# Optimization experiments

Hardware: AMD Instinct MI355X
Metric: run time of the kernel (lower is better)

Reference implementation:

```python
import math
import jax, jax.numpy as jnp
import numpy as np

B, S, H, N = 2, 2048, 2048, 16
HN = H // N
ALPHA = 32.0
MASK_VALUE = 10000.0


def setup_inputs() -> dict:
    key = jax.random.key(0)
    k1, k2, k3, k4, k5 = jax.random.split(key, 5)
    hidden_states = jax.random.normal(k1, (B, S, H), dtype=jnp.float32)
    # causal (left-to-right) multiplicative mask, broadcastable to [b, n, s, s]
    ltor_mask = jnp.tril(jnp.ones((S, S), dtype=jnp.float32))[None, None, :, :]
    # torch Linear params: y = x @ W.T + b
    w_qkv = jax.random.normal(k2, (3 * H, H), dtype=jnp.float32) * (1.0 / math.sqrt(H))
    b_qkv = jnp.zeros((3 * H,), dtype=jnp.float32)
    w_dense = jax.random.normal(k3, (H, H), dtype=jnp.float32) * (1.0 / math.sqrt(H))
    b_dense = jnp.zeros((H,), dtype=jnp.float32)
    return {"hidden_states": hidden_states, "ltor_mask": ltor_mask,
            "w_qkv": w_qkv, "b_qkv": b_qkv, "w_dense": w_dense, "b_dense": b_dense}


def reference(hidden_states, ltor_mask, w_qkv, b_qkv, w_dense, b_dense):
    b, s, h = hidden_states.shape
    # fused qkv projection
    qkv = hidden_states @ w_qkv.T + b_qkv                       # [b, s, 3h]
    q, k, v = jnp.split(qkv, 3, axis=-1)

    def heads(t):  # [b, s, h] -> [b, n, s, hn]
        return t.reshape(b, s, N, HN).transpose(0, 2, 1, 3)

    q, k, v = heads(q), heads(k), heads(v)
    # cogview pb_relax: scale query before matmul
    scores = jnp.einsum('bnsd,bntd->bnst', q / math.sqrt(HN), k)  # [b, n, s, s]
    m = ltor_mask[:, :, -s:]
    scores = scores * m - MASK_VALUE * (1.0 - m)
    # pb_relax max stabilization: per (batch, head) global max of scores/alpha
    scaled = scores / ALPHA
    maxes = jax.lax.stop_gradient(jnp.max(scaled, axis=(-2, -1), keepdims=True))
    scores = (scaled - maxes) * ALPHA
    probs = jax.nn.softmax(scores, axis=-1)
    ctx = jnp.einsum('bnst,bntd->bnsd', probs, v)                # [b, n, s, hn]
    ctx = ctx.transpose(0, 2, 1, 3).reshape(b, s, h)
    out = ctx @ w_dense.T + b_dense
    return out
```

## Files before the change

### kernel.cpp

```cpp
#include <hip/hip_runtime.h>

typedef __bf16 bf16_t;
typedef __bf16 bf16x8 __attribute__((ext_vector_type(8)));
typedef __bf16 bf16x4 __attribute__((ext_vector_type(4)));
typedef float f32x4 __attribute__((ext_vector_type(4)));

#define MFMA16(a, b, c) __builtin_amdgcn_mfma_f32_16x16x32_bf16((a), (b), (c), 0, 0, 0)

__device__ __forceinline__ void gload_lds16(const void* g, void* l) {
  __builtin_amdgcn_global_load_lds(
      (__attribute__((address_space(1))) void*)(g),
      (__attribute__((address_space(3))) void*)(l), 16, 0, 0);
}

__device__ __forceinline__ void block_bar() {
  asm volatile("" ::: "memory");
  __builtin_amdgcn_s_barrier();
  asm volatile("" ::: "memory");
}

__global__ __launch_bounds__(256) void cvt_f32_bf16(const float* __restrict__ in,
                                                    bf16_t* __restrict__ out, int n4) {
  int i = blockIdx.x * 256 + threadIdx.x;
  if (i >= n4) return;
  float4 v = ((const float4*)in)[i];
  bf16x4 o;
  o[0] = (bf16_t)v.x; o[1] = (bf16_t)v.y; o[2] = (bf16_t)v.z; o[3] = (bf16_t)v.w;
  ((bf16x4*)out)[i] = o;
}

template <int EPI>
__global__ __launch_bounds__(256) void gemm_bt(
    const bf16_t* __restrict__ A, const bf16_t* __restrict__ Bw,
    const float* __restrict__ bias,
    void* __restrict__ o0, void* __restrict__ o1, void* __restrict__ o2,
    int M, int N, int K) {
  __shared__ __attribute__((aligned(16))) bf16_t As[2][128][32];
  __shared__ __attribute__((aligned(16))) bf16_t Bs[2][128][32];
  const int tid = threadIdx.x;
  const int lane = tid & 63, wave = tid >> 6;
  const int wr = (wave >> 1) * 64, wc = (wave & 1) * 64;
  const int l15 = lane & 15, l4 = lane >> 4;
  const int bm = blockIdx.y * 128, bn = blockIdx.x * 128;

  f32x4 acc[4][4];
#pragma unroll
  for (int i = 0; i < 4; ++i)
#pragma unroll
    for (int j = 0; j < 4; ++j)
#pragma unroll
      for (int r = 0; r < 4; ++r) acc[i][j][r] = 0.0f;

  const int r0 = tid >> 2;
  const int co = (tid & 3) * 8;
  const bf16_t* gA = A + (size_t)(bm + r0) * K + co;
  const bf16_t* gB = Bw + (size_t)(bn + r0) * K + co;

  const int nt = K >> 5;

  gload_lds16(gA, &As[0][r0][co]);
  gload_lds16(gA + (size_t)64 * K, &As[0][r0 + 64][co]);
  gload_lds16(gB, &Bs[0][r0][co]);
  gload_lds16(gB + (size_t)64 * K, &Bs[0][r0 + 64][co]);

#pragma unroll 1
  for (int t = 0; t < nt; ++t) {
    const int cb = t & 1;
    if (t + 1 < nt) {
      const int kk = (t + 1) << 5;
      const int nb = cb ^ 1;
      gload_lds16(gA + kk, &As[nb][r0][co]);
      gload_lds16(gA + kk + (size_t)64 * K, &As[nb][r0 + 64][co]);
      gload_lds16(gB + kk, &Bs[nb][r0][co]);
      gload_lds16(gB + kk + (size_t)64 * K, &Bs[nb][r0 + 64][co]);
      asm volatile("s_waitcnt vmcnt(4)" ::: "memory");
    } else {
      asm volatile("s_waitcnt vmcnt(0)" ::: "memory");
    }
    block_bar();
    bf16x8 a[4], b[4];
#pragma unroll
    for (int i = 0; i < 4; ++i) a[i] = *(const bf16x8*)(&As[cb][wr + i * 16 + l15][l4 * 8]);
#pragma unroll
    for (int j = 0; j < 4; ++j) b[j] = *(const bf16x8*)(&Bs[cb][wc + j * 16 + l15][l4 * 8]);
#pragma unroll
    for (int i = 0; i < 4; ++i)
#pragma unroll
      for (int j = 0; j < 4; ++j) acc[i][j] = MFMA16(a[i], b[j], acc[i][j]);
    block_bar();
  }

  if (EPI == 0) {
    bf16_t* qb = (bf16_t*)o0;
    bf16_t* kb = (bf16_t*)o1;
    bf16_t* vtb = (bf16_t*)o2;
    const int which = bn >> 11;
    const int head = (bn & 2047) >> 7;
#pragma unroll
    for (int i = 0; i < 4; ++i)
#pragma unroll
      for (int j = 0; j < 4; ++j)
#pragma unroll
        for (int r = 0; r < 4; ++r) {
          int m = bm + wr + i * 16 + l4 * 4 + r;
          int n = bn + wc + j * 16 + l15;
          float v = acc[i][j][r] + bias[n];
          int b = m >> 11, s = m & 2047;
          int d = n & 127;
          size_t hb = (size_t)(b * 16 + head);
          if (which == 0) {
            v *= 0.08838834764831845f;
            qb[(hb * 2048 + s) * 128 + d] = (bf16_t)v;
          } else if (which == 1) {
            kb[(hb * 2048 + s) * 128 + d] = (bf16_t)v;
          } else {
            vtb[(hb * 128 + d) * 2048 + s] = (bf16_t)v;
          }
        }
  } else {
    float* O = (float*)o0;
#pragma unroll
    for (int i = 0; i < 4; ++i)
#pragma unroll
      for (int j = 0; j < 4; ++j)
#pragma unroll
        for (int r = 0; r < 4; ++r) {
          int m = bm + wr + i * 16 + l4 * 4 + r;
          int n = bn + wc + j * 16 + l15;
          O[(size_t)m * N + n] = acc[i][j][r] + bias[n];
        }
  }
}

__global__ __launch_bounds__(512) void attn_kernel(
    const bf16_t* __restrict__ qbuf, const bf16_t* __restrict__ kbuf,
    const bf16_t* __restrict__ vtbuf, bf16_t* __restrict__ ctx) {
  __shared__ __attribute__((aligned(16))) bf16_t Ks[2][64][128];
  __shared__ __attribute__((aligned(16))) bf16_t Vts[2][128][64];
  __shared__ __attribute__((aligned(16))) bf16_t Ps[8][16][64];

  const int tid = threadIdx.x, lane = tid & 63, w = tid >> 6;
  const int l15 = lane & 15, l4 = lane >> 4;
  const int hb = blockIdx.y;
  const size_t hoff = (size_t)hb * 2048 * 128;
  const bf16_t* qh = qbuf + hoff;
  const bf16_t* kh = kbuf + hoff;
  const bf16_t* vh = vtbuf + hoff;
  const int b = hb >> 4, head = hb & 15;

  const int kr0 = tid >> 4, ks0 = tid & 15;
  const int vr0 = tid >> 3, vs0 = tid & 7;

  int buf = 0;

#pragma unroll 1
  for (int phase = 0; phase < 2; ++phase) {
    const int qt = phase == 0 ? blockIdx.x : 15 - blockIdx.x;
    const int q0 = qt * 128;
    const int nt = 2 * qt + 2;

    bf16x8 qa[4];
#pragma unroll
    for (int ks = 0; ks < 4; ++ks)
      qa[ks] = *(const bf16x8*)(qh + (size_t)(q0 + w * 16 + l15) * 128 + ks * 32 + l4 * 8);

    f32x4 accO[8];
#pragma unroll
    for (int df = 0; df < 8; ++df)
#pragma unroll
      for (int r = 0; r < 4; ++r) accO[df][r] = 0.0f;
    float mrow[4], lrow[4];
#pragma unroll
    for (int r = 0; r < 4; ++r) { mrow[r] = -1e30f; lrow[r] = 0.0f; }

    {
      const int kv0 = 0;
#pragma unroll
      for (int it = 0; it < 2; ++it) {
        int row = kr0 + it * 32, sch = ks0 ^ (row & 7);
        gload_lds16(kh + (size_t)(kv0 + row) * 128 + sch * 8, &Ks[buf][row][ks0 * 8]);
      }
#pragma unroll
      for (int it = 0; it < 2; ++it) {
        int row = vr0 + it * 64, sch = vs0 ^ (row & 7);
        gload_lds16(vh + (size_t)row * 2048 + kv0 + sch * 8, &Vts[buf][row][vs0 * 8]);
      }
    }

#pragma unroll 1
    for (int t = 0; t < nt; ++t) {
      const int kv0 = t * 64;
      if (t + 1 < nt) {
        const int kvn = (t + 1) * 64;
        const int nb = buf ^ 1;
#pragma unroll
        for (int it = 0; it < 2; ++it) {
          int row = kr0 + it * 32, sch = ks0 ^ (row & 7);
          gload_lds16(kh + (size_t)(kvn + row) * 128 + sch * 8, &Ks[nb][row][ks0 * 8]);
        }
#pragma unroll
        for (int it = 0; it < 2; ++it) {
          int row = vr0 + it * 64, sch = vs0 ^ (row & 7);
          gload_lds16(vh + (size_t)row * 2048 + kvn + sch * 8, &Vts[nb][row][vs0 * 8]);
        }
        asm volatile("s_waitcnt vmcnt(4)" ::: "memory");
      } else {
        asm volatile("s_waitcnt vmcnt(0)" ::: "memory");
      }
      block_bar();

      const bool active = (kv0 <= q0 + w * 16 + 15);
      if (active) {
        f32x4 sc[4];
#pragma unroll
        for (int nf = 0; nf < 4; ++nf) {
#pragma unroll
          for (int r = 0; r < 4; ++r) sc[nf][r] = 0.0f;
          int row = nf * 16 + l15;
#pragma unroll
          for (int ks = 0; ks < 4; ++ks) {
            int ch = (ks * 4 + l4) ^ (row & 7);
            bf16x8 kf = *(const bf16x8*)(&Ks[buf][row][ch * 8]);
            sc[nf] = MFMA16(qa[ks], kf, sc[nf]);
          }
        }

        if (kv0 + 63 > q0 + w * 16) {
#pragma unroll
          for (int nf = 0; nf < 4; ++nf)
#pragma unroll
            for (int r = 0; r < 4; ++r) {
              int qi = q0 + w * 16 + l4 * 4 + r;
              int kv = kv0 + nf * 16 + l15;
              if (kv > qi) sc[nf][r] = -1e30f;
            }
        }

        float tmax[4];
#pragma unroll
        for (int r = 0; r < 4; ++r)
          tmax[r] = fmaxf(fmaxf(sc[0][r], sc[1][r]), fmaxf(sc[2][r], sc[3][r]));
#pragma unroll
        for (int msk = 1; msk <= 8; msk <<= 1)
#pragma unroll
          for (int r = 0; r < 4; ++r)
            tmax[r] = fmaxf(tmax[r], __shfl_xor(tmax[r], msk, 64));

        bool defer = __all(tmax[0] <= mrow[0] + 8.0f && tmax[1] <= mrow[1] + 8.0f &&
                           tmax[2] <= mrow[2] + 8.0f && tmax[3] <= mrow[3] + 8.0f);
        if (!defer) {
          float scl[4];
#pragma unroll
          for (int r = 0; r < 4; ++r) {
            float mn = fmaxf(mrow[r], tmax[r]);
            scl[r] = __expf(mrow[r] - mn);
            mrow[r] = mn;
            lrow[r] *= scl[r];
          }
#pragma unroll
          for (int df = 0; df < 8; ++df)
#pragma unroll
            for (int r = 0; r < 4; ++r) accO[df][r] *= scl[r];
        }

        float rsum[4];
#pragma unroll
        for (int r = 0; r < 4; ++r) {
          float s0 = 0.0f;
#pragma unroll
          for (int nf = 0; nf < 4; ++nf) {
            float p = __expf(sc[nf][r] - mrow[r]);
            sc[nf][r] = p;
            s0 += p;
          }
          rsum[r] = s0;
        }
#pragma unroll
        for (int msk = 1; msk <= 8; msk <<= 1)
#pragma unroll
          for (int r = 0; r < 4; ++r) rsum[r] += __shfl_xor(rsum[r], msk, 64);
#pragma unroll
        for (int r = 0; r < 4; ++r) lrow[r] += rsum[r];

#pragma unroll
        for (int nf = 0; nf < 4; ++nf)
#pragma unroll
          for (int r = 0; r < 4; ++r) {
            int qi = l4 * 4 + r;
            int kv = nf * 16 + l15;
            int ch = (kv >> 3) ^ (qi & 7);
            Ps[w][qi][ch * 8 + (kv & 7)] = (bf16_t)sc[nf][r];
          }

        bf16x8 pa[2];
#pragma unroll
        for (int k2 = 0; k2 < 2; ++k2) {
          int ch = (k2 * 4 + l4) ^ (l15 & 7);
          pa[k2] = *(const bf16x8*)(&Ps[w][l15][ch * 8]);
        }
#pragma unroll
        for (int df = 0; df < 8; ++df) {
          int row = df * 16 + l15;
#pragma unroll
          for (int k2 = 0; k2 < 2; ++k2) {
            int ch = (k2 * 4 + l4) ^ (row & 7);
            bf16x8 vf = *(const bf16x8*)(&Vts[buf][row][ch * 8]);
            accO[df] = MFMA16(pa[k2], vf, accO[df]);
          }
        }
      }
      block_bar();
      buf ^= 1;
    }

    float inv[4];
#pragma unroll
    for (int r = 0; r < 4; ++r) inv[r] = 1.0f / lrow[r];
#pragma unroll
    for (int df = 0; df < 8; ++df)
#pragma unroll
      for (int r = 0; r < 4; ++r) {
        int s = q0 + w * 16 + l4 * 4 + r;
        int col = head * 128 + df * 16 + l15;
        ctx[((size_t)(b * 2048 + s)) * 2048 + col] = (bf16_t)(accO[df][r] * inv[r]);
      }
  }
}

extern "C" void kernel_launch(void* const* d_in, const int* in_sizes, int n_in,
                              void* d_out, int out_size, void* d_ws, size_t ws_size,
                              hipStream_t stream) {
  const float* hs = (const float*)d_in[0];
  const float* w_qkv = (const float*)d_in[2];
  const float* b_qkv = (const float*)d_in[3];
  const float* w_dense = (const float*)d_in[4];
  const float* b_dense = (const float*)d_in[5];
  float* out = (float*)d_out;

  const size_t SZ_HS = (size_t)4096 * 2048;
  const size_t SZ_WQKV = (size_t)6144 * 2048;
  const size_t SZ_WD = (size_t)2048 * 2048;
  const size_t SZ_H = (size_t)32 * 2048 * 128;

  char* ws = (char*)d_ws;
  bf16_t* A_ = (bf16_t*)ws;
  bf16_t* B_ = (bf16_t*)(ws + 2 * SZ_HS);
  bf16_t* Q_ = (bf16_t*)(ws + 2 * (SZ_HS + SZ_WQKV));
  bf16_t* K_ = Q_ + SZ_H;
  bf16_t* V_ = K_ + SZ_H;

  cvt_f32_bf16<<<(int)(SZ_HS / 4 / 256), 256, 0, stream>>>(hs, A_, (int)(SZ_HS / 4));
  cvt_f32_bf16<<<(int)(SZ_WQKV / 4 / 256), 256, 0, stream>>>(w_qkv, B_, (int)(SZ_WQKV / 4));

  gemm_bt<0><<<dim3(48, 32), 256, 0, stream>>>(A_, B_, b_qkv, Q_, K_, V_, 4096, 6144, 2048);

  cvt_f32_bf16<<<(int)(SZ_WD / 4 / 256), 256, 0, stream>>>(w_dense, A_, (int)(SZ_WD / 4));

  attn_kernel<<<dim3(8, 32), 512, 0, stream>>>(Q_, K_, V_, B_);

  gemm_bt<1><<<dim3(16, 32), 256, 0, stream>>>(B_, A_, b_dense, out, nullptr, nullptr,
                                               4096, 2048, 2048);
}
```

Measured before the change: 431.6 us.

## Use 256x256 tiled QKV GEMM with swizzled LDS and interleaved prefetch

Replaces the 128x128 QKV projection GEMM with a dedicated 512-thread kernel using 256x256 output tiles and a K step of 64. It uses XOR-swizzled LDS to avoid bank conflicts and staggers next-tile global-to-LDS loads between MFMA phases, with s_setprio raised around the MFMA bursts. The intent is more data reuse per loaded byte and better overlap of memory with compute. The cost is higher register and LDS use (128KB LDS), which lowers occupancy, and 384 blocks, which may leave the GPU's CUs unevenly loaded.

Measured after the change: 440.2 us. +2.0%, slower.

```diff
diff --git a/kernel.cpp b/kernel.cpp
--- a/kernel.cpp
+++ b/kernel.cpp
@@ -29,11 +29,149 @@
   ((bf16x4*)out)[i] = o;
 }
 
-template <int EPI>
-__global__ __launch_bounds__(256) void gemm_bt(
+__global__ __launch_bounds__(512) void gemm_qkv_256(
     const bf16_t* __restrict__ A, const bf16_t* __restrict__ Bw,
     const float* __restrict__ bias,
-    void* __restrict__ o0, void* __restrict__ o1, void* __restrict__ o2,
+    bf16_t* __restrict__ qb, bf16_t* __restrict__ kb, bf16_t* __restrict__ vtb,
+    int M, int N, int K) {
+  __shared__ __attribute__((aligned(16))) bf16_t As[2][256][64];
+  __shared__ __attribute__((aligned(16))) bf16_t Bs[2][256][64];
+  const int tid = threadIdx.x;
+  const int lane = tid & 63;
+  const int w = tid >> 6;
+  const int wm = w >> 2, wn = w & 3;
+  const int l15 = lane & 15, l4 = lane >> 4;
+  const int bm = blockIdx.y * 256, bn = blockIdx.x * 256;
+
+  f32x4 acc[8][4];
+#pragma unroll
+  for (int i = 0; i < 8; ++i)
+#pragma unroll
+    for (int j = 0; j < 4; ++j)
+#pragma unroll
+      for (int r = 0; r < 4; ++r) acc[i][j][r] = 0.0f;
+
+  const int srow = tid >> 3;
+  const int schk = tid & 7;
+
+  auto stageA = [&](int q, int ti, int i) {
+    int r = (i << 6) + srow;
+    int cl = (schk ^ (r & 7)) << 3;
+    gload_lds16(A + (size_t)(bm + r) * K + (ti << 6) + cl, &As[q][r][schk << 3]);
+  };
+  auto stageB = [&](int q, int ti, int i) {
+    int r = (i << 6) + srow;
+    int cl = (schk ^ (r & 7)) << 3;
+    gload_lds16(Bw + (size_t)(bn + r) * K + (ti << 6) + cl, &Bs[q][r][schk << 3]);
+  };
+  auto afrag = [&](int p, int mf, int ks) -> bf16x8 {
+    int row = wm * 128 + mf * 16 + l15;
+    int ch = ((ks << 2) | l4) ^ (row & 7);
+    return *(const bf16x8*)(&As[p][row][ch << 3]);
+  };
+  auto bfrag = [&](int p, int nf, int ks) -> bf16x8 {
+    int row = wn * 64 + nf * 16 + l15;
+    int ch = ((ks << 2) | l4) ^ (row & 7);
+    return *(const bf16x8*)(&Bs[p][row][ch << 3]);
+  };
+
+  const int nt = K >> 6;
+
+#pragma unroll
+  for (int i = 0; i < 4; ++i) stageA(0, 0, i);
+#pragma unroll
+  for (int i = 0; i < 4; ++i) stageB(0, 0, i);
+
+  bf16x8 afr[4], bfr[4];
+
+#pragma unroll 1
+  for (int t = 0; t < nt; ++t) {
+    const int p = t & 1, q = p ^ 1;
+    const bool pf = (t + 1 < nt);
+    asm volatile("s_waitcnt vmcnt(0)" ::: "memory");
+    block_bar();
+
+#pragma unroll
+    for (int n = 0; n < 4; ++n) bfr[n] = bfrag(p, n, 0);
+#pragma unroll
+    for (int j = 0; j < 4; ++j) afr[j] = afrag(p, j, 0);
+    if (pf) { stageA(q, t + 1, 0); stageA(q, t + 1, 1); }
+    block_bar();
+    __builtin_amdgcn_s_setprio(1);
+#pragma unroll
+    for (int j = 0; j < 4; ++j)
+#pragma unroll
+      for (int n = 0; n < 4; ++n) acc[j][n] = MFMA16(afr[j], bfr[n], acc[j][n]);
+    __builtin_amdgcn_s_setprio(0);
+    block_bar();
+
+#pragma unroll
+    for (int j = 0; j < 4; ++j) afr[j] = afrag(p, 4 + j, 0);
+    if (pf) { stageA(q, t + 1, 2); stageA(q, t + 1, 3); }
+    block_bar();
+    __builtin_amdgcn_s_setprio(1);
+#pragma unroll
+    for (int j = 0; j < 4; ++j)
+#pragma unroll
+      for (int n = 0; n < 4; ++n) acc[4 + j][n] = MFMA16(afr[j], bfr[n], acc[4 + j][n]);
+    __builtin_amdgcn_s_setprio(0);
+    block_bar();
+
+#pragma unroll
+    for (int n = 0; n < 4; ++n) bfr[n] = bfrag(p, n, 1);
+#pragma unroll
+    for (int j = 0; j < 4; ++j) afr[j] = afrag(p, j, 1);
+    if (pf) { stageB(q, t + 1, 0); stageB(q, t + 1, 1); }
+    block_bar();
+    __builtin_amdgcn_s_setprio(1);
+#pragma unroll
+    for (int j = 0; j < 4; ++j)
+#pragma unroll
+      for (int n = 0; n < 4; ++n) acc[j][n] = MFMA16(afr[j], bfr[n], acc[j][n]);
+    __builtin_amdgcn_s_setprio(0);
+    block_bar();
+
+#pragma unroll
+    for (int j = 0; j < 4; ++j) afr[j] = afrag(p, 4 + j, 1);
+    if (pf) { stageB(q, t + 1, 2); stageB(q, t + 1, 3); }
+    block_bar();
+    __builtin_amdgcn_s_setprio(1);
+#pragma unroll
+    for (int j = 0; j < 4; ++j)
+#pragma unroll
+      for (int n = 0; n < 4; ++n) acc[4 + j][n] = MFMA16(afr[j], bfr[n], acc[4 + j][n]);
+    __builtin_amdgcn_s_setprio(0);
+    block_bar();
+  }
+
+  const int which = bn >> 11;
+#pragma unroll
+  for (int mf = 0; mf < 8; ++mf)
+#pragma unroll
+    for (int nf = 0; nf < 4; ++nf)
+#pragma unroll
+      for (int r = 0; r < 4; ++r) {
+        int m = bm + wm * 128 + mf * 16 + l4 * 4 + r;
+        int n = bn + wn * 64 + nf * 16 + l15;
+        float v = acc[mf][nf][r] + bias[n];
+        int b = m >> 11, s = m & 2047;
+        int d = n & 127;
+        int head = (n & 2047) >> 7;
+        size_t hb = (size_t)(b * 16 + head);
+        if (which == 0) {
+          v *= 0.08838834764831845f;
+          qb[(hb * 2048 + s) * 128 + d] = (bf16_t)v;
+        } else if (which == 1) {
+          kb[(hb * 2048 + s) * 128 + d] = (bf16_t)v;
+        } else {
+          vtb[(hb * 128 + d) * 2048 + s] = (bf16_t)v;
+        }
+      }
+}
+
+__global__ __launch_bounds__(256) void gemm_bt_dense(
+    const bf16_t* __restrict__ A, const bf16_t* __restrict__ Bw,
+    const float* __restrict__ bias, float* __restrict__ O,
     int M, int N, int K) {
   __shared__ __attribute__((aligned(16))) bf16_t As[2][128][32];
   __shared__ __attribute__((aligned(16))) bf16_t Bs[2][128][32];
@@ -90,46 +228,16 @@
     block_bar();
   }
 
-  if (EPI == 0) {
-    bf16_t* qb = (bf16_t*)o0;
-    bf16_t* kb = (bf16_t*)o1;
-    bf16_t* vtb = (bf16_t*)o2;
-    const int which = bn >> 11;
-    const int head = (bn & 2047) >> 7;
-#pragma unroll
-    for (int i = 0; i < 4; ++i)
-#pragma unroll
-      for (int j = 0; j < 4; ++j)
-#pragma unroll
-        for (int r = 0; r < 4; ++r) {
-          int m = bm + wr + i * 16 + l4 * 4 + r;
-          int n = bn + wc + j * 16 + l15;
-          float v = acc[i][j][r] + bias[n];
-          int b = m >> 11, s = m & 2047;
-          int d = n & 127;
-          size_t hb = (size_t)(b * 16 + head);
-          if (which == 0) {
-            v *= 0.08838834764831845f;
-            qb[(hb * 2048 + s) * 128 + d] = (bf16_t)v;
-          } else if (which == 1) {
-            kb[(hb * 2048 + s) * 128 + d] = (bf16_t)v;
-          } else {
-            vtb[(hb * 128 + d) * 2048 + s] = (bf16_t)v;
-          }
-        }
-  } else {
-    float* O = (float*)o0;
-#pragma unroll
-    for (int i = 0; i < 4; ++i)
-#pragma unroll
-      for (int j = 0; j < 4; ++j)
-#pragma unroll
-        for (int r = 0; r < 4; ++r) {
-          int m = bm + wr + i * 16 + l4 * 4 + r;
-          int n = bn + wc + j * 16 + l15;
-          O[(size_t)m * N + n] = acc[i][j][r] + bias[n];
-        }
-  }
+#pragma unroll
+  for (int i = 0; i < 4; ++i)
+#pragma unroll
+    for (int j = 0; j < 4; ++j)
+#pragma unroll
+      for (int r = 0; r < 4; ++r) {
+        int m = bm + wr + i * 16 + l4 * 4 + r;
+        int n = bn + wc + j * 16 + l15;
+        O[(size_t)m * N + n] = acc[i][j][r] + bias[n];
+      }
 }
 
 __global__ __launch_bounds__(512) void attn_kernel(
@@ -352,12 +460,11 @@
   cvt_f32_bf16<<<(int)(SZ_HS / 4 / 256), 256, 0, stream>>>(hs, A_, (int)(SZ_HS / 4));
   cvt_f32_bf16<<<(int)(SZ_WQKV / 4 / 256), 256, 0, stream>>>(w_qkv, B_, (int)(SZ_WQKV / 4));
 
-  gemm_bt<0><<<dim3(48, 32), 256, 0, stream>>>(A_, B_, b_qkv, Q_, K_, V_, 4096, 6144, 2048);
+  gemm_qkv_256<<<dim3(24, 16), 512, 0, stream>>>(A_, B_, b_qkv, Q_, K_, V_, 4096, 6144, 2048);
 
   cvt_f32_bf16<<<(int)(SZ_WD / 4 / 256), 256, 0, stream>>>(w_dense, A_, (int)(SZ_WD / 4));
 
   attn_kernel<<<dim3(8, 32), 512, 0, stream>>>(Q_, K_, V_, B_);
 
-  gemm_bt<1><<<dim3(16, 32), 256, 0, stream>>>(B_, A_, b_dense, out, nullptr, nullptr,
-                                               4096, 2048, 2048);
-}
+  gemm_bt_dense<<<dim3(16, 32), 256, 0, stream>>>(B_, A_, b_dense, out, 4096, 2048, 2048);
+}
```
